# Performance work log

Hardware: AMD Instinct MI355X
Metric: run time of the kernel (lower is better)

## Reference

```python
import jax, jax.numpy as jnp
import numpy as np

# ---- model constants (stand-ins for the Qiskit circuit / SparsePauliOp) ----
Q = 20           # qubits
L = 4            # ansatz layers: RY on every qubit, then ring of CZ
R = 24           # tensor-ring bond rank (init kwarg `rank`)
P = Q * L        # number of circuit parameters
CDT = jnp.complex64

_CZ = jnp.asarray(np.diag([1.0, 1.0, 1.0, -1.0]).reshape(2, 2, 2, 2), CDT)

# Observable H = 0.8*Z0 Z1 + 0.5*Z3 (Z/I-only -> 'efficient' expectation path)
_TERMS = [(0.8, (0, 1)), (0.5, (3,))]
_ZDIAG = jnp.asarray([1.0, -1.0], CDT)


def _init_cores():
    # |0...0> product state embedded in rank-R ring cores (identity bonds),
    # plus a tiny fixed perturbation so truncated-SVD singular values are
    # generic (keeps jax.vjp through SVD well-conditioned).
    rng = np.random.default_rng(0)
    cores = []
    for _ in range(Q):
        c = np.zeros((R, 2, R), np.complex64)
        c[:, 0, :] = np.eye(R, dtype=np.complex64)
        c = c + 1e-2 * (rng.standard_normal((R, 2, R))
                        + 1j * rng.standard_normal((R, 2, R))).astype(np.complex64)
        cores.append(jnp.asarray(c))
    return cores

_INIT_CORES = _init_cores()


def _apply_1q(core, U2):
    # core: (R, 2, R); U2: (2, 2) acting on the physical index
    return jnp.einsum('ts,asb->atb', U2, core)


def _apply_2q(ci, cj, U4):
    # merge neighboring ring cores, apply 4x4 gate, split via truncated SVD
    theta = jnp.einsum('asb,btc->astc', ci, cj)        # (R,2,2,R)
    theta = jnp.einsum('uvst,astc->auvc', U4, theta)   # gate on physical (s,t)
    M = theta.reshape(2 * R, 2 * R)
    Uu, s, Vh = jnp.linalg.svd(M, full_matrices=False)
    sr = jnp.sqrt(s[:R]).astype(CDT)                   # split sqrt(s) both ways
    ci_new = (Uu[:, :R] * sr[None, :]).reshape(R, 2, R)
    cj_new = (sr[:, None] * Vh[:R, :]).reshape(R, 2, R)
    return ci_new, cj_new


def _ring_ev(cores, zqubits):
    # <psi| (prod_i D_i) |psi> for diagonal D_i in {I, Z}; trace-closed ring.
    # Boundary M[p,q,b,r]: p/b = ket open/running bonds, q/r = bra bonds.
    eye = jnp.eye(R, dtype=CDT)
    M = jnp.einsum('ab,cd->acbd', eye, eye)            # (R,R,R,R)
    zset = set(zqubits)
    for i in range(Q):
        A = cores[i]
        Ad = A * _ZDIAG[None, :, None] if i in zset else A
        T = jnp.einsum('pqbr,bsc->pqrsc', M, Ad)       # contract ket bond, 2R^5
        M = jnp.einsum('pqrsc,rsd->pqcd', T, jnp.conj(A))  # bra bond + phys
    return jnp.einsum('pqpq->', M)                     # close the ring trace


def _forward(params):
    cores = list(_INIT_CORES)
    idx = 0
    for _ in range(L):
        for q in range(Q):
            half = params[idx] * 0.5
            idx += 1
            c, s = jnp.cos(half), jnp.sin(half)
            U2 = jnp.stack([jnp.stack([c, -s]), jnp.stack([s, c])]).astype(CDT)
            cores[q] = _apply_1q(cores[q], U2)
        for q in range(Q):                              # ring of CZ (wraps)
            j = (q + 1) % Q
            cores[q], cores[j] = _apply_2q(cores[q], cores[j], _CZ)
    norm = jnp.real(_ring_ev(cores, ()))
    ev = sum(c * jnp.real(_ring_ev(cores, zq)) for c, zq in _TERMS)
    return (ev / norm).astype(jnp.float32)


def setup_inputs() -> dict:
    key = jax.random.key(0)
    params = jax.random.normal(key, (P,), dtype=jnp.float32)
    return {"params": params}


def reference(params):
    return _forward(params)
```

## Files before the change

kernel.cpp:

```cpp
#include <hip/hip_runtime.h>
#include <cstdint>
#include <cmath>
#include <cstring>


#define RK 24
#define NQ 20
#define NLAY 4
#define NCOL 48
#define AS 49
#define NSWEEP 8
#define NTHR 384
#define CORE_ELEMS (RK * 2 * RK)
#define M4 (RK * RK * RK * RK)

namespace npyrng {

struct Pcg64 {
  unsigned __int128 state, inc;
  static inline unsigned __int128 mult() {
    return (((unsigned __int128)0x2360ED051FC65DA4ull) << 64) |
           0x4385DF649FCCF645ull;
  }
  inline void step() { state = state * mult() + inc; }
  inline uint64_t next64() {
    step();
    uint64_t hi = (uint64_t)(state >> 64), lo = (uint64_t)state;
    uint64_t v = hi ^ lo;
    unsigned r = (unsigned)(state >> 122);
    return (v >> r) | (v << ((64u - r) & 63u));
  }
  inline double nextDouble() {
    return (double)(next64() >> 11) * (1.0 / 9007199254740992.0);
  }
};

struct ZigTables {
  uint64_t ki[256];
  double wi[256], fi[256];
};

static void build_tables(ZigTables& T) {
  const double NR = 3.6541528853610088;
  const double PI = 3.14159265358979323846;
  double f = std::exp(-0.5 * NR * NR);
  double V = NR * f + std::sqrt(PI / 2.0) * std::erfc(NR / std::sqrt(2.0));
  const double m1 = 4503599627370496.0;
  double q = V / f;
  T.ki[0] = (uint64_t)((NR / q) * m1);
  T.ki[1] = 0;
  T.wi[0] = q / m1;
  T.wi[255] = NR / m1;
  T.fi[0] = 1.0;
  T.fi[255] = f;
  double tn = NR;
  for (int i = 254; i >= 1; --i) {
    double dn = std::sqrt(-2.0 * std::log(V / tn + std::exp(-0.5 * tn * tn)));
    T.ki[i + 1] = (uint64_t)((dn / tn) * m1);
    T.fi[i] = std::exp(-0.5 * dn * dn);
    T.wi[i] = dn / m1;
    tn = dn;
  }
}

static double std_normal(Pcg64& g, const ZigTables& T) {
  const double NR = 3.6541528853610088;
  const double INV_NR = 0.27366123732975828;
  for (;;) {
    uint64_t r = g.next64();
    int idx = (int)(r & 0xff);
    r >>= 8;
    int sign = (int)(r & 1);
    uint64_t rabs = (r >> 1) & 0x000fffffffffffffull;
    double x = (double)rabs * T.wi[idx];
    if (sign) x = -x;
    if (rabs < T.ki[idx]) return x;
    if (idx == 0) {
      for (;;) {
        double xx = -INV_NR * std::log1p(-g.nextDouble());
        double yy = -std::log1p(-g.nextDouble());
        if (yy + yy > xx * xx)
          return ((rabs >> 8) & 1) ? -(NR + xx) : (NR + xx);
      }
    } else {
      if ((T.fi[idx - 1] - T.fi[idx]) * g.nextDouble() + T.fi[idx] <
          std::exp(-0.5 * x * x))
        return x;
    }
  }
}

static void seed_pcg64_numpy0(Pcg64& g) {
  const uint32_t INIT_A = 0x43b0d7e5u, MULT_A = 0x931e8875u;
  const uint32_t INIT_B = 0x8b51f9ddu, MULT_B = 0x58f38dedu;
  const uint32_t MIX_L = 0xca01f9ddu, MIX_R = 0x4973f715u;
  uint32_t pool[4];
  uint32_t hc = INIT_A;
  auto hashf = [&](uint32_t value) -> uint32_t {
    value ^= hc;
    hc *= MULT_A;
    value *= hc;
    value ^= value >> 16;
    return value;
  };
  auto mixf = [&](uint32_t x, uint32_t y) -> uint32_t {
    uint32_t r = x * MIX_L - y * MIX_R;
    r ^= r >> 16;
    return r;
  };
  uint32_t entropy0 = 0u;
  for (int i = 0; i < 4; ++i) pool[i] = hashf(i < 1 ? entropy0 : 0u);
  for (int s = 0; s < 4; ++s)
    for (int d = 0; d < 4; ++d)
      if (s != d) pool[d] = mixf(pool[d], hashf(pool[s]));
  uint32_t w[8];
  uint32_t hb = INIT_B;
  for (int i = 0; i < 8; ++i) {
    uint32_t dv = pool[i & 3];
    dv ^= hb;
    hb *= MULT_B;
    dv *= hb;
    dv ^= dv >> 16;
    w[i] = dv;
  }
  uint64_t v0 = (uint64_t)w[0] | ((uint64_t)w[1] << 32);
  uint64_t v1 = (uint64_t)w[2] | ((uint64_t)w[3] << 32);
  uint64_t v2 = (uint64_t)w[4] | ((uint64_t)w[5] << 32);
  uint64_t v3 = (uint64_t)w[6] | ((uint64_t)w[7] << 32);
  unsigned __int128 initstate = (((unsigned __int128)v0) << 64) | v1;
  unsigned __int128 initseq = (((unsigned __int128)v2) << 64) | v3;
  g.state = 0;
  g.inc = (initseq << 1) | 1;
  g.step();
  g.state += initstate;
  g.step();
}

}

static float h_cores[NQ * CORE_ELEMS * 2];

static void fill_host_cores() {
  npyrng::Pcg64 g;
  npyrng::seed_pcg64_numpy0(g);
  npyrng::ZigTables T;
  npyrng::build_tables(T);
  double re[CORE_ELEMS], im[CORE_ELEMS];
  for (int core = 0; core < NQ; ++core) {
    for (int t = 0; t < CORE_ELEMS; ++t) re[t] = npyrng::std_normal(g, T);
    for (int t = 0; t < CORE_ELEMS; ++t) im[t] = npyrng::std_normal(g, T);
    for (int o = 0; o < CORE_ELEMS; ++o) {
      int a = o / (2 * RK);
      int s = (o / RK) & 1;
      int b = o % RK;
      float baser = (s == 0 && a == b) ? 1.0f : 0.0f;
      float nr = (float)re[o], ni = (float)im[o];
      h_cores[(core * CORE_ELEMS + o) * 2 + 0] = baser + 0.01f * nr;
      h_cores[(core * CORE_ELEMS + o) * 2 + 1] = 0.01f * ni;
    }
  }
}

__device__ __forceinline__ float row_reduce16(float x) {
  int v;
  v = __builtin_amdgcn_update_dpp(0, __float_as_int(x), 0x128, 0xf, 0xf, false);
  x += __int_as_float(v);
  v = __builtin_amdgcn_update_dpp(0, __float_as_int(x), 0x124, 0xf, 0xf, false);
  x += __int_as_float(v);
  v = __builtin_amdgcn_update_dpp(0, __float_as_int(x), 0x122, 0xf, 0xf, false);
  x += __int_as_float(v);
  v = __builtin_amdgcn_update_dpp(0, __float_as_int(x), 0x121, 0xf, 0xf, false);
  x += __int_as_float(v);
  return x;
}

__global__ __launch_bounds__(NTHR) void evolve_kernel(
    const float* __restrict__ params, float2* __restrict__ cores) {
  __shared__ float2 A[NCOL * AS];
  __shared__ float2 M0[NCOL * NCOL];
  __shared__ float nrm[NCOL];
  __shared__ float sig2[NCOL];
  __shared__ int keepSrc[RK];
  __shared__ float csbuf[NQ * 2];
  __shared__ int sweepFlag;

  const int tid = threadIdx.x;
  const int team = tid >> 4;
  const int sub = tid & 15;

  for (int layer = 0; layer < NLAY; ++layer) {
    if (tid < NQ) {
      float half = 0.5f * params[layer * NQ + tid];
      csbuf[2 * tid] = cosf(half);
      csbuf[2 * tid + 1] = sinf(half);
    }
    __syncthreads();
    for (int o = tid; o < NQ * RK * RK; o += NTHR) {
      int qq = o / (RK * RK);
      int ab = o % (RK * RK);
      int a = ab / RK, b = ab % RK;
      float ch = csbuf[2 * qq], sh = csbuf[2 * qq + 1];
      float2* base = cores + qq * CORE_ELEMS;
      float2 c0 = base[(a * 2 + 0) * RK + b];
      float2 c1 = base[(a * 2 + 1) * RK + b];
      base[(a * 2 + 0) * RK + b] =
          make_float2(ch * c0.x - sh * c1.x, ch * c0.y - sh * c1.y);
      base[(a * 2 + 1) * RK + b] =
          make_float2(sh * c0.x + ch * c1.x, sh * c0.y + ch * c1.y);
    }
    __syncthreads();

    for (int qg = 0; qg < NQ; ++qg) {
      int jg = (qg + 1) % NQ;
      const float2* ci = cores + qg * CORE_ELEMS;
      const float2* cj = cores + jg * CORE_ELEMS;

      for (int o = tid; o < CORE_ELEMS; o += NTHR) {
        M0[o] = ci[o];
        M0[CORE_ELEMS + o] = cj[o];
      }
      __syncthreads();

      float2 mv[6];
      {
        int k = 0;
        for (int o = tid; o < NCOL * NCOL; o += NTHR, ++k) {
          int col = o / NCOL, row = o % NCOL;
          int a = row >> 1, s = row & 1;
          int t = col / RK, cc = col % RK;
          float accx = 0.f, accy = 0.f;
          for (int b = 0; b < RK; ++b) {
            float2 x = M0[(a * 2 + s) * RK + b];
            float2 y = M0[CORE_ELEMS + (b * 2 + t) * RK + cc];
            accx += x.x * y.x - x.y * y.y;
            accy += x.x * y.y + x.y * y.x;
          }
          if (s == 1 && t == 1) { accx = -accx; accy = -accy; }
          mv[k] = make_float2(accx, accy);
        }
      }
      __syncthreads();
      {
        int k = 0;
        for (int o = tid; o < NCOL * NCOL; o += NTHR, ++k) {
          int col = o / NCOL, row = o % NCOL;
          A[col * AS + row] = mv[k];
          M0[col * NCOL + row] = mv[k];
        }
      }
      __syncthreads();

      for (int col = team; col < NCOL; col += 24) {
        float2 x0 = A[col * AS + sub];
        float2 x1 = A[col * AS + sub + 16];
        float2 x2 = A[col * AS + sub + 32];
        float nn = x0.x * x0.x + x0.y * x0.y + x1.x * x1.x + x1.y * x1.y +
                   x2.x * x2.x + x2.y * x2.y;
        nn = row_reduce16(nn);
        if (sub == 0) nrm[col] = nn;
      }
      __syncthreads();

      for (int sw = 0; sw < NSWEEP; ++sw) {
        if (tid == 0) sweepFlag = 0;
        int p = (team == 0) ? 47 : team;
        int qc = (team == 0) ? 0 : (47 - team);
        __syncthreads();
        for (int r = 0; r < 47; ++r) {
          const int pb_ = p * AS, qb_ = qc * AS;
          float na = nrm[p];
          float nb = nrm[qc];
          float2 ap0 = A[pb_ + sub], ap1 = A[pb_ + sub + 16],
                 ap2 = A[pb_ + sub + 32];
          float2 aq0 = A[qb_ + sub], aq1 = A[qb_ + sub + 16],
                 aq2 = A[qb_ + sub + 32];
          float pr = ap0.x * aq0.x + ap0.y * aq0.y + ap1.x * aq1.x +
                     ap1.y * aq1.y + ap2.x * aq2.x + ap2.y * aq2.y;
          float pi = ap0.x * aq0.y - ap0.y * aq0.x + ap1.x * aq1.y -
                     ap1.y * aq1.x + ap2.x * aq2.y - ap2.y * aq2.x;
          pr = row_reduce16(pr);
          pi = row_reduce16(pi);
          float m2 = pr * pr + pi * pi;
          bool want = (sub == 0) && (m2 > 1e-7f * na * nb);
          unsigned long long bal = __ballot(want);
          if ((tid & 63) == 0 && bal != 0ull) sweepFlag = 1;
          if (m2 > 1e-30f && m2 > 1e-14f * na * nb) {
            float inv_m = rsqrtf(m2);
            float zr = pr * inv_m, zi = pi * inv_m;
            float tau = (na - nb) * 0.5f * inv_m;
            float tt = 1.f / (fabsf(tau) + sqrtf(1.f + tau * tau));
            if (tau < 0.f) tt = -tt;
            float cc_ = rsqrtf(1.f + tt * tt);
            float ss = tt * cc_;
#define ROT_PAIR(xp, xq, outp, outq)                                       \
  {                                                                        \
    float zqr = zr * xq.x + zi * xq.y;                                     \
    float zqi = zr * xq.y - zi * xq.x;                                     \
    float2 npv = make_float2(cc_ * xp.x + ss * zqr, cc_ * xp.y + ss * zqi);\
    float zpr = zr * xp.x - zi * xp.y;                                     \
    float zpi = zr * xp.y + zi * xp.x;                                     \
    float2 nqv = make_float2(cc_ * xq.x - ss * zpr, cc_ * xq.y - ss * zpi);\
    outp = npv;                                                            \
    outq = nqv;                                                            \
  }
            ROT_PAIR(ap0, aq0, A[pb_ + sub], A[qb_ + sub]);
            ROT_PAIR(ap1, aq1, A[pb_ + sub + 16], A[qb_ + sub + 16]);
            ROT_PAIR(ap2, aq2, A[pb_ + sub + 32], A[qb_ + sub + 32]);
#undef ROT_PAIR
            if (sub == 0) {
              float m = m2 * inv_m;
              float c2 = cc_ * cc_, s2 = ss * ss;
              float cs2m = 2.f * cc_ * ss * m;
              nrm[p] = c2 * na + s2 * nb + cs2m;
              nrm[qc] = s2 * na + c2 * nb - cs2m;
            }
          }
          if (team != 0) p = (p + 1 == 47) ? 0 : p + 1;
          qc = (qc + 1 == 47) ? 0 : qc + 1;
          __syncthreads();
        }
        int f = sweepFlag;
        __syncthreads();
        if (f == 0) break;
      }

      for (int col = team; col < NCOL; col += 24) {
        float2 x0 = A[col * AS + sub];
        float2 x1 = A[col * AS + sub + 16];
        float2 x2 = A[col * AS + sub + 32];
        float nn = x0.x * x0.x + x0.y * x0.y + x1.x * x1.x + x1.y * x1.y +
                   x2.x * x2.x + x2.y * x2.y;
        nn = row_reduce16(nn);
        if (sub == 0) sig2[col] = nn;
      }
      __syncthreads();

      if (tid < NCOL) {
        float mine = sig2[tid];
        int rk = 0;
        for (int kx = 0; kx < NCOL; ++kx) {
          float o = sig2[kx];
          if (o > mine || (o == mine && kx < tid)) ++rk;
        }
        if (rk < RK) keepSrc[rk] = tid;
      }
      __syncthreads();

      for (int o = tid; o < RK * NCOL; o += NTHR) {
        int bn = o / NCOL;
        int row = o % NCOL;
        int src = keepSrc[bn];
        float sg = sqrtf(sig2[src]);
        float su = rsqrtf(fmaxf(sg, 1e-30f));
        float2 x = A[src * AS + row];
        cores[qg * CORE_ELEMS + row * RK + bn] =
            make_float2(x.x * su, x.y * su);
      }
      for (int o = tid; o < RK * NCOL; o += NTHR) {
        int bn = o / NCOL;
        int col = o % NCOL;
        int src = keepSrc[bn];
        float s2 = fmaxf(sig2[src], 1e-30f);
        float scale = rsqrtf(s2) * rsqrtf(sqrtf(s2));
        float accx = 0.f, accy = 0.f;
        const float2* ac = &A[src * AS];
        const float2* mc = &M0[col * NCOL];
#pragma unroll 8
        for (int rr = 0; rr < NCOL; ++rr) {
          float2 u = ac[rr];
          float2 mm = mc[rr];
          accx += u.x * mm.x + u.y * mm.y;
          accy += u.x * mm.y - u.y * mm.x;
        }
        cores[jg * CORE_ELEMS + bn * (2 * RK) + col] =
            make_float2(accx * scale, accy * scale);
      }
      __syncthreads();
    }
  }
}

__global__ __launch_bounds__(256) void init_m_kernel(float2* __restrict__ mb) {
  int i = blockIdx.x * 256 + threadIdx.x;
  if (i >= M4) return;
  int r = i % RK;
  int b = (i / RK) % RK;
  int q = (i / (RK * RK)) % RK;
  int p = i / (RK * RK * RK);
  mb[i] = make_float2((p == b && q == r) ? 1.f : 0.f, 0.f);
}

__global__ __launch_bounds__(256) void ring_step_kernel(
    const float2* __restrict__ Min, float2* __restrict__ Mout,
    const float2* __restrict__ cores, int qubit, int zmask) {
  __shared__ float2 Msh[RK * RK];
  __shared__ float2 Ash[CORE_ELEMS];
  __shared__ float2 Tsh[RK * 2 * RK];
  const int pq = blockIdx.x;
  const float zs = ((zmask >> qubit) & 1) ? -1.f : 1.f;
  const float2* minpq = Min + (size_t)pq * (RK * RK);
  for (int o = threadIdx.x; o < RK * RK; o += 256) Msh[o] = minpq[o];
  const float2* Ac = cores + qubit * CORE_ELEMS;
  for (int o = threadIdx.x; o < CORE_ELEMS; o += 256) Ash[o] = Ac[o];
  __syncthreads();
  for (int o = threadIdx.x; o < RK * 2 * RK; o += 256) {
    int r = o / (2 * RK);
    int sc = o % (2 * RK);
    int s = sc / RK, c = sc % RK;
    float sgn = (s == 1) ? zs : 1.f;
    float accx = 0.f, accy = 0.f;
#pragma unroll 8
    for (int b = 0; b < RK; ++b) {
      float2 m = Msh[b * RK + r];
      float2 a = Ash[(b * 2 + s) * RK + c];
      accx += m.x * a.x - m.y * a.y;
      accy += m.x * a.y + m.y * a.x;
    }
    Tsh[o] = make_float2(accx * sgn, accy * sgn);
  }
  __syncthreads();
  float2* moutpq = Mout + (size_t)pq * (RK * RK);
  for (int o = threadIdx.x; o < RK * RK; o += 256) {
    int c = o / RK, d = o % RK;
    float accx = 0.f, accy = 0.f;
    for (int r = 0; r < RK; ++r)
#pragma unroll
      for (int s = 0; s < 2; ++s) {
        float2 t = Tsh[r * (2 * RK) + s * RK + c];
        float2 a = Ash[(r * 2 + s) * RK + d];
        accx += t.x * a.x + t.y * a.y;
        accy += t.y * a.x - t.x * a.y;
      }
    moutpq[o] = make_float2(accx, accy);
  }
}

__global__ __launch_bounds__(256) void trace_kernel(
    const float2* __restrict__ mb, float* __restrict__ dst) {
  __shared__ float sh[4];
  float tr = 0.f;
  for (int o = threadIdx.x; o < RK * RK; o += 256) {
    int p = o / RK, q = o % RK;
    tr += mb[(size_t)o * (RK * RK) + p * RK + q].x;
  }
  for (int d = 1; d < 64; d <<= 1) tr += __shfl_xor(tr, d);
  int wave = threadIdx.x >> 6, lane = threadIdx.x & 63;
  if (lane == 0) sh[wave] = tr;
  __syncthreads();
  if (threadIdx.x == 0) dst[0] = sh[0] + sh[1] + sh[2] + sh[3];
}

__global__ void final_kernel(const float* __restrict__ trs,
                             float* __restrict__ out) {
  if (threadIdx.x == 0)
    out[0] = (0.8f * trs[1] + 0.5f * trs[2]) / trs[0];
}

extern "C" void kernel_launch(void* const* d_in, const int* in_sizes, int n_in,
                              void* d_out, int out_size, void* d_ws,
                              size_t ws_size, hipStream_t stream) {
  const float* params = (const float*)d_in[0];
  float* out = (float*)d_out;
  char* ws = (char*)d_ws;

  const size_t CORES_BYTES = sizeof(h_cores);
  const size_t MB_BYTES = (size_t)M4 * sizeof(float2);
  float2* cores = (float2*)ws;
  float2* B0 = (float2*)(ws + CORES_BYTES);
  float2* B1 = (float2*)(ws + CORES_BYTES + MB_BYTES);
  float2* B2 = (float2*)(ws + CORES_BYTES + 2 * MB_BYTES);
  float* tr_ws = (float*)(ws + CORES_BYTES + 3 * MB_BYTES);

  fill_host_cores();
  hipMemcpyAsync(cores, h_cores, CORES_BYTES, hipMemcpyHostToDevice, stream);

  evolve_kernel<<<1, NTHR, 0, stream>>>(params, cores);

  init_m_kernel<<<(M4 + 255) / 256, 256, 0, stream>>>(B0);
  for (int qb = 4; qb < 20; ++qb) {
    const float2* src = ((qb - 4) & 1) ? B1 : B0;
    float2* dst = ((qb - 4) & 1) ? B0 : B1;
    ring_step_kernel<<<RK * RK, 256, 0, stream>>>(src, dst, cores, qb, 0);
  }
  for (int e = 0; e < 3; ++e) {
    int zm = (e == 0) ? 0 : (e == 1 ? 3 : 8);
    ring_step_kernel<<<RK * RK, 256, 0, stream>>>(B0, B1, cores, 0, zm);
    ring_step_kernel<<<RK * RK, 256, 0, stream>>>(B1, B2, cores, 1, zm);
    ring_step_kernel<<<RK * RK, 256, 0, stream>>>(B2, B1, cores, 2, zm);
    ring_step_kernel<<<RK * RK, 256, 0, stream>>>(B1, B2, cores, 3, zm);
    trace_kernel<<<1, 256, 0, stream>>>(B2, tr_ws + e);
  }
  final_kernel<<<1, 64, 0, stream>>>(tr_ws, out);
}
```

Baseline: 20.50 ms.

## Use hierarchical block-pair Jacobi ordering to cut block-wide barriers per sweep

Replaces the flat round-robin Jacobi ordering (47 rounds, each ending in a block barrier) with a two-level tournament. The 48 columns are grouped into 12 blocks of 4, and each wave owns a block pair for 11 outer rounds. Inside a round the wave does 7 inner rotation steps over its 8 columns using only wave-level barriers, so block-wide syncthreads drop from 47 to 11 per sweep. The convergence flag is now gathered once per sweep. The rotation arithmetic is unchanged, but the pair visiting order differs, which may change how many sweeps are needed to converge.

```diff
diff --git a/kernel.cpp b/kernel.cpp
--- a/kernel.cpp
+++ b/kernel.cpp
@@ -185,8 +185,11 @@
   __shared__ int sweepFlag;
 
   const int tid = threadIdx.x;
-  const int team = tid >> 4;
+  const int wv = tid >> 6;
+  const int slot = (tid >> 4) & 3;
   const int sub = tid & 15;
+
+  if (tid == 0) sweepFlag = 0;
 
   for (int layer = 0; layer < NLAY; ++layer) {
     if (tid < NQ) {
@@ -250,7 +253,7 @@
       }
       __syncthreads();
 
-      for (int col = team; col < NCOL; col += 24) {
+      for (int col = (tid >> 4); col < NCOL; col += 24) {
         float2 x0 = A[col * AS + sub];
         float2 x1 = A[col * AS + sub + 16];
         float2 x2 = A[col * AS + sub + 32];
@@ -261,70 +264,87 @@
       }
       __syncthreads();
 
-      for (int sw = 0; sw < NSWEEP; ++sw) {
-        if (tid == 0) sweepFlag = 0;
-        int p = (team == 0) ? 47 : team;
-        int qc = (team == 0) ? 0 : (47 - team);
-        __syncthreads();
-        for (int r = 0; r < 47; ++r) {
-          const int pb_ = p * AS, qb_ = qc * AS;
-          float na = nrm[p];
-          float nb = nrm[qc];
-          float2 ap0 = A[pb_ + sub], ap1 = A[pb_ + sub + 16],
-                 ap2 = A[pb_ + sub + 32];
-          float2 aq0 = A[qb_ + sub], aq1 = A[qb_ + sub + 16],
-                 aq2 = A[qb_ + sub + 32];
-          float pr = ap0.x * aq0.x + ap0.y * aq0.y + ap1.x * aq1.x +
-                     ap1.y * aq1.y + ap2.x * aq2.x + ap2.y * aq2.y;
-          float pi = ap0.x * aq0.y - ap0.y * aq0.x + ap1.x * aq1.y -
-                     ap1.y * aq1.x + ap2.x * aq2.y - ap2.y * aq2.x;
-          pr = row_reduce16(pr);
-          pi = row_reduce16(pi);
-          float m2 = pr * pr + pi * pi;
-          bool want = (sub == 0) && (m2 > 1e-7f * na * nb);
-          unsigned long long bal = __ballot(want);
-          if ((tid & 63) == 0 && bal != 0ull) sweepFlag = 1;
-          if (m2 > 1e-30f && m2 > 1e-14f * na * nb) {
-            float inv_m = rsqrtf(m2);
-            float zr = pr * inv_m, zi = pi * inv_m;
-            float tau = (na - nb) * 0.5f * inv_m;
-            float tt = 1.f / (fabsf(tau) + sqrtf(1.f + tau * tau));
-            if (tau < 0.f) tt = -tt;
-            float cc_ = rsqrtf(1.f + tt * tt);
-            float ss = tt * cc_;
-#define ROT_PAIR(xp, xq, outp, outq)                                       \
-  {                                                                        \
-    float zqr = zr * xq.x + zi * xq.y;                                     \
-    float zqi = zr * xq.y - zi * xq.x;                                     \
-    float2 npv = make_float2(cc_ * xp.x + ss * zqr, cc_ * xp.y + ss * zqi);\
-    float zpr = zr * xp.x - zi * xp.y;                                     \
-    float zpi = zr * xp.y + zi * xp.x;                                     \
-    float2 nqv = make_float2(cc_ * xq.x - ss * zpr, cc_ * xq.y - ss * zpi);\
-    outp = npv;                                                            \
-    outq = nqv;                                                            \
-  }
-            ROT_PAIR(ap0, aq0, A[pb_ + sub], A[qb_ + sub]);
-            ROT_PAIR(ap1, aq1, A[pb_ + sub + 16], A[qb_ + sub + 16]);
-            ROT_PAIR(ap2, aq2, A[pb_ + sub + 32], A[qb_ + sub + 32]);
+      for (int ss = 0; ss < NSWEEP; ++ss) {
+        bool myActive = false;
+        for (int sr = 0; sr < 11; ++sr) {
+          int qa, qb;
+          if (wv == 0) {
+            qa = 11; qb = sr;
+          } else {
+            qa = sr + wv; if (qa >= 11) qa -= 11;
+            qb = sr + 11 - wv; if (qb >= 11) qb -= 11;
+          }
+          const int qa4 = qa * 4, qb4 = qb * 4;
+          for (int m = 0; m < 7; ++m) {
+            int pA, pB;
+            if (slot == 0) {
+              pA = 7; pB = m;
+            } else {
+              pA = m + slot; if (pA >= 7) pA -= 7;
+              pB = m + 7 - slot; if (pB >= 7) pB -= 7;
+            }
+            int gp = (pA < 4) ? (qa4 + pA) : (qb4 + pA - 4);
+            int gq = (pB < 4) ? (qa4 + pB) : (qb4 + pB - 4);
+            const int pb_ = gp * AS, qb_ = gq * AS;
+            float na = nrm[gp];
+            float nb = nrm[gq];
+            float2 ap0 = A[pb_ + sub], ap1 = A[pb_ + sub + 16],
+                   ap2 = A[pb_ + sub + 32];
+            float2 aq0 = A[qb_ + sub], aq1 = A[qb_ + sub + 16],
+                   aq2 = A[qb_ + sub + 32];
+            float pr = ap0.x * aq0.x + ap0.y * aq0.y + ap1.x * aq1.x +
+                       ap1.y * aq1.y + ap2.x * aq2.x + ap2.y * aq2.y;
+            float pi = ap0.x * aq0.y - ap0.y * aq0.x + ap1.x * aq1.y -
+                       ap1.y * aq1.x + ap2.x * aq2.y - ap2.y * aq2.x;
+            pr = row_reduce16(pr);
+            pi = row_reduce16(pi);
+            float m2 = pr * pr + pi * pi;
+            myActive = myActive || (m2 > 1e-7f * na * nb);
+            if (m2 > 1e-30f && m2 > 1e-14f * na * nb) {
+              float inv_m = rsqrtf(m2);
+              float zr = pr * inv_m, zi = pi * inv_m;
+              float tau = (na - nb) * 0.5f * inv_m;
+              float tt = 1.f / (fabsf(tau) + sqrtf(1.f + tau * tau));
+              if (tau < 0.f) tt = -tt;
+              float cc_ = rsqrtf(1.f + tt * tt);
+              float ss_ = tt * cc_;
+#define ROT_PAIR(xp, xq, outp, outq)                                        \
+  {                                                                         \
+    float zqr = zr * xq.x + zi * xq.y;                                      \
+    float zqi = zr * xq.y - zi * xq.x;                                      \
+    float2 npv = make_float2(cc_ * xp.x + ss_ * zqr, cc_ * xp.y + ss_ * zqi);\
+    float zpr = zr * xp.x - zi * xp.y;                                      \
+    float zpi = zr * xp.y + zi * xp.x;                                      \
+    float2 nqv = make_float2(cc_ * xq.x - ss_ * zpr, cc_ * xq.y - ss_ * zpi);\
+    outp = npv;                                                             \
+    outq = nqv;                                                             \
+  }
+              ROT_PAIR(ap0, aq0, A[pb_ + sub], A[qb_ + sub]);
+              ROT_PAIR(ap1, aq1, A[pb_ + sub + 16], A[qb_ + sub + 16]);
+              ROT_PAIR(ap2, aq2, A[pb_ + sub + 32], A[qb_ + sub + 32]);
 #undef ROT_PAIR
-            if (sub == 0) {
-              float m = m2 * inv_m;
-              float c2 = cc_ * cc_, s2 = ss * ss;
-              float cs2m = 2.f * cc_ * ss * m;
-              nrm[p] = c2 * na + s2 * nb + cs2m;
-              nrm[qc] = s2 * na + c2 * nb - cs2m;
+              if (sub == 0) {
+                float mg = m2 * inv_m;
+                float c2 = cc_ * cc_, s2 = ss_ * ss_;
+                float cs2m = 2.f * cc_ * ss_ * mg;
+                nrm[gp] = c2 * na + s2 * nb + cs2m;
+                nrm[gq] = s2 * na + c2 * nb - cs2m;
+              }
             }
+            __builtin_amdgcn_wave_barrier();
           }
-          if (team != 0) p = (p + 1 == 47) ? 0 : p + 1;
-          qc = (qc + 1 == 47) ? 0 : qc + 1;
           __syncthreads();
         }
+        unsigned long long bal = __ballot(myActive);
+        if ((tid & 63) == 0 && bal != 0ull) sweepFlag = 1;
+        __syncthreads();
         int f = sweepFlag;
         __syncthreads();
+        if (tid == 0) sweepFlag = 0;
         if (f == 0) break;
       }
 
-      for (int col = team; col < NCOL; col += 24) {
+      for (int col = (tid >> 4); col < NCOL; col += 24) {
         float2 x0 = A[col * AS + sub];
         float2 x1 = A[col * AS + sub + 16];
         float2 x2 = A[col * AS + sub + 32];
```

New measurement: 29.54 ms. +44.1%, slower.
